# Kernel optimization log

Measured on AMD Instinct MI355X. Metric: run time of the kernel, lower is better.

The kernel has to match this reference:

```python
import jax, jax.numpy as jnp
import numpy as np

H_IN = 1024
H_OUT = 1024
P = 512
DT_MIN = 0.004
DT_MAX = 0.1
STEP_RESCALE = 1.0
MIN_NEG = 1e-3
EPS_LAM = 1e-6
EPS_DIV = 1e-9
CLIP_MAX = 20.0


def _hippo_lambda_raw(p):
    # Mirrors TorchS5.__init__ HiPPO-LegS-style symmetric init.
    idx = np.arange(p, dtype=np.float64)
    Pv = np.sqrt(1.0 + 2.0 * idx)
    A = np.tril(Pv[:, None] * Pv[None, :]) - np.diag(idx)
    A = -A
    Pr = np.sqrt(idx + 0.5)
    S = A + Pr[:, None] * Pr[None, :]
    S_sym = 0.5 * (S + S.T)
    eig = np.linalg.eigvalsh(S_sym).astype(np.float32)
    lambda_init = -np.clip(np.abs(eig), 1e-3, None)
    raw = -np.log(np.expm1(np.clip(-lambda_init, 1e-6, None)))
    return jnp.asarray(raw, dtype=jnp.float32)


def setup_inputs() -> dict:
    key = jax.random.key(0)
    ku, kt, kb, kc = jax.random.split(key, 4)
    Bsz, L = 16, 1024
    u = jax.random.normal(ku, (Bsz, L, H_IN), dtype=jnp.float32)
    timesteps = jax.random.uniform(kt, (Bsz, L), dtype=jnp.float32)
    Lambda_raw = _hippo_lambda_raw(P)
    log_step_init = 0.5 * (np.log(DT_MIN) + np.log(DT_MAX))
    log_step = jnp.full((P,), log_step_init, dtype=jnp.float32)
    # kaiming_uniform_(a=sqrt(5)) -> U(-1/sqrt(fan_in), 1/sqrt(fan_in))
    Bmat = jax.random.uniform(kb, (P, H_IN), dtype=jnp.float32,
                              minval=-1.0, maxval=1.0) / np.sqrt(H_IN)
    Cmat = jax.random.uniform(kc, (H_OUT, P), dtype=jnp.float32,
                              minval=-1.0, maxval=1.0) / np.sqrt(P)
    Dvec = jnp.zeros((H_IN,), dtype=jnp.float32)  # H_in == H_out path
    return {"u": u, "timesteps": timesteps, "Lambda_raw": Lambda_raw,
            "log_step": log_step, "B": Bmat, "C": Cmat, "D": Dvec}


def reference(u, timesteps, Lambda_raw, log_step, B, C, D):
    # u: [B,L,H_in], timesteps: [B,L]
    Bu = jnp.einsum('ph,blh->blp', B, u)                      # [B,L,P]
    step_vec = STEP_RESCALE * jnp.exp(log_step)               # [P]
    Lam = -(jax.nn.softplus(Lambda_raw) + MIN_NEG)            # [P]
    Delta = jnp.maximum(step_vec[None, None, :] * timesteps[..., None], 0.0)
    A_bar = jnp.exp(jnp.minimum(Lam[None, None, :] * Delta, CLIP_MAX))
    # zoh gamma: (exp(Lam*Delta)-1)/Lam, fallback Delta near Lam=0
    gamma = jnp.where(jnp.abs(Lam)[None, None, :] > EPS_LAM,
                      (A_bar - 1.0) / Lam[None, None, :], Delta)
    b_seq = gamma * Bu
    A_cum = jnp.cumprod(A_bar, axis=1)                        # [B,L,P]
    z = b_seq / (A_cum + EPS_DIV)
    s = jnp.cumsum(z, axis=1)
    x_seq = A_cum * s
    ys = jnp.einsum('hp,blp->blh', C, x_seq) + D * u          # [B,L,H_out]
    return ys
```

## Files before the change

kernel.cpp:

```cpp
#include <hip/hip_runtime.h>
#include <cstdint>
#include <cstddef>

#define H_IN   1024
#define H_OUTD 1024
#define PDIM   512
#define BSZ    16
#define LSEQ   1024
#define BLM    (BSZ * LSEQ)
#define CCH    32
#define CLEN   32

typedef __bf16 bf16_t;
typedef __bf16 bf16x8 __attribute__((ext_vector_type(8)));
typedef float  floatx4 __attribute__((ext_vector_type(4)));

__device__ __forceinline__ unsigned short f2bf(float f) {
    unsigned u = __float_as_uint(f);
    u = u + 0x7fffu + ((u >> 16) & 1u);
    return (unsigned short)(u >> 16);
}
__device__ __forceinline__ float bf2f(unsigned short s) {
    return __uint_as_float((unsigned)s << 16);
}

__device__ __forceinline__ void gl_lds16(const void* g, void* l) {
    __builtin_amdgcn_global_load_lds(
        (const __attribute__((address_space(1))) void*)g,
        (__attribute__((address_space(3))) void*)l, 16, 0, 0);
}

#define NU4 (BLM * H_IN / 4)
#define NB4 (PDIM * H_IN / 4)
#define NC4 (H_OUTD * PDIM / 4)
__global__ void setup_kernel(const float* __restrict__ Lraw,
                             const float* __restrict__ lstep,
                             float* __restrict__ stepv,
                             float* __restrict__ lamv,
                             const float4* __restrict__ Usrc,
                             ushort4* __restrict__ Udst,
                             const float4* __restrict__ Bsrc,
                             ushort4* __restrict__ Bdst,
                             const float4* __restrict__ Csrc,
                             ushort4* __restrict__ Cdst) {
    const int gid = blockIdx.x * 256 + threadIdx.x;
    if (gid < PDIM) {
        stepv[gid] = expf(lstep[gid]);
        float x = Lraw[gid];
        float sp = fmaxf(x, 0.0f) + log1pf(expf(-fabsf(x)));
        lamv[gid] = -(sp + 1e-3f);
    }
    if (gid < NU4) {
        float4 v = Usrc[gid];
        ushort4 o;
        o.x = f2bf(v.x); o.y = f2bf(v.y); o.z = f2bf(v.z); o.w = f2bf(v.w);
        Udst[gid] = o;
    } else {
        const int g2 = gid - NU4;
        if (g2 < NB4) {
            float4 v = Bsrc[g2];
            ushort4 o;
            o.x = f2bf(v.x); o.y = f2bf(v.y); o.z = f2bf(v.z); o.w = f2bf(v.w);
            Bdst[g2] = o;
        } else if (g2 < NB4 + NC4) {
            const int g3 = g2 - NB4;
            float4 v = Csrc[g3];
            ushort4 o;
            o.x = f2bf(v.x); o.y = f2bf(v.y); o.z = f2bf(v.z); o.w = f2bf(v.w);
            Cdst[g3] = o;
        }
    }
}

template<int GXL>
__global__ __launch_bounds__(256, 4)
void gemm1_bm64(const bf16_t* __restrict__ A, const bf16_t* __restrict__ Bm,
                unsigned short* __restrict__ Cb, int M, int N, int K) {
    constexpr int ABUF = 64 * 32;
    constexpr int BBUF = 128 * 32;
    __shared__ bf16_t As[2 * ABUF];
    __shared__ bf16_t Bs[2 * BBUF];

    const int i     = blockIdx.x;
    const int n_blk = (i >> 3) & ((1 << GXL) - 1);
    const int m_blk = ((i >> (3 + GXL)) << 3) | (i & 7);
    const int m0    = m_blk * 64;
    const int n0    = n_blk << 7;

    const int tid  = threadIdx.x;
    const int lane = tid & 63;
    const int w    = tid >> 6;
    const int wm   = (w & 1) * 32;
    const int wn   = (w >> 1) * 64;
    const int r16  = lane & 15;
    const int q    = lane >> 4;
    const int fsw  = (q ^ (r16 & 3)) << 3;

    const int srow = lane >> 2;
    const int seg  = (lane & 3) ^ (srow & 3);
    const int aro  = w * 16;
    const int bc0  = w * 32;

    const bf16_t* gA  = A  + (size_t)(m0 + aro + srow) * K + seg * 8;
    const bf16_t* gB0 = Bm + (size_t)(n0 + bc0 + srow) * K + seg * 8;
    const bf16_t* gB1 = Bm + (size_t)(n0 + bc0 + 16 + srow) * K + seg * 8;
    bf16_t* lA  = &As[aro * 32];
    bf16_t* lB0 = &Bs[bc0 * 32];
    bf16_t* lB1 = &Bs[(bc0 + 16) * 32];

    floatx4 acc[2][4] = {};

    gl_lds16(gA,  lA);
    gl_lds16(gB0, lB0);
    gl_lds16(gB1, lB1);
    __syncthreads();

    int cur = 0;
    for (int k0 = 0; k0 < K; k0 += 32) {
        const int nxt = cur ^ 1;
        if (k0 + 32 < K) {
            gl_lds16(gA  + k0 + 32, lA  + nxt * ABUF);
            gl_lds16(gB0 + k0 + 32, lB0 + nxt * BBUF);
            gl_lds16(gB1 + k0 + 32, lB1 + nxt * BBUF);
        }

        const bf16_t* rA = As + cur * ABUF;
        const bf16_t* rB = Bs + cur * BBUF;
        bf16x8 af[2], bfr[4];
#pragma unroll
        for (int ii = 0; ii < 2; ++ii)
            af[ii]  = *(const bf16x8*)&rA[(wm + ii * 16 + r16) * 32 + fsw];
#pragma unroll
        for (int ii = 0; ii < 4; ++ii)
            bfr[ii] = *(const bf16x8*)&rB[(wn + ii * 16 + r16) * 32 + fsw];
#pragma unroll
        for (int mi = 0; mi < 2; ++mi)
#pragma unroll
            for (int ni = 0; ni < 4; ++ni)
                acc[mi][ni] = __builtin_amdgcn_mfma_f32_16x16x32_bf16(
                    af[mi], bfr[ni], acc[mi][ni], 0, 0, 0);

        __syncthreads();
        cur = nxt;
    }

#pragma unroll
    for (int mi = 0; mi < 2; ++mi) {
#pragma unroll
        for (int e = 0; e < 4; ++e) {
            const int m = m0 + wm + mi * 16 + q * 4 + e;
#pragma unroll
            for (int ni = 0; ni < 4; ++ni) {
                const int n = n0 + wn + ni * 16 + r16;
                Cb[(size_t)m * N + n] = f2bf(acc[mi][ni][e]);
            }
        }
    }
}

template<int GXL>
__global__ __launch_bounds__(256, 4)
void gemm2_nt(const bf16_t* __restrict__ A, const bf16_t* __restrict__ Bm,
              float* __restrict__ Cf, int M, int N, int K,
              const float* __restrict__ Dv, const float* __restrict__ U32) {
    __shared__ bf16_t As[2 * 4096];
    __shared__ bf16_t Bs[2 * 4096];

    const int i     = blockIdx.x;
    const int n_blk = (i >> 3) & ((1 << GXL) - 1);
    const int m_blk = ((i >> (3 + GXL)) << 3) | (i & 7);
    const int m0    = m_blk << 7;
    const int n0    = n_blk << 7;

    const int tid  = threadIdx.x;
    const int lane = tid & 63;
    const int w    = tid >> 6;
    const int wm   = (w & 1) << 6;
    const int wn   = (w >> 1) << 6;
    const int r16  = lane & 15;
    const int q    = lane >> 4;
    const int fsw  = (q ^ (r16 & 3)) << 3;

    const int srow = lane >> 2;
    const int seg  = (lane & 3) ^ (srow & 3);
    const int c0   = w * 32;
    const int c1   = c0 + 16;

    const bf16_t* gA0 = A  + (size_t)(m0 + c0 + srow) * K + seg * 8;
    const bf16_t* gA1 = A  + (size_t)(m0 + c1 + srow) * K + seg * 8;
    const bf16_t* gB0 = Bm + (size_t)(n0 + c0 + srow) * K + seg * 8;
    const bf16_t* gB1 = Bm + (size_t)(n0 + c1 + srow) * K + seg * 8;
    bf16_t* lA0 = &As[c0 * 32];
    bf16_t* lA1 = &As[c1 * 32];
    bf16_t* lB0 = &Bs[c0 * 32];
    bf16_t* lB1 = &Bs[c1 * 32];

    floatx4 acc[4][4] = {};

    gl_lds16(gA0, lA0);
    gl_lds16(gA1, lA1);
    gl_lds16(gB0, lB0);
    gl_lds16(gB1, lB1);
    __syncthreads();

    int cur = 0;
    for (int k0 = 0; k0 < K; k0 += 32) {
        const int nxt = cur ^ 1;
        if (k0 + 32 < K) {
            gl_lds16(gA0 + k0 + 32, lA0 + nxt * 4096);
            gl_lds16(gA1 + k0 + 32, lA1 + nxt * 4096);
            gl_lds16(gB0 + k0 + 32, lB0 + nxt * 4096);
            gl_lds16(gB1 + k0 + 32, lB1 + nxt * 4096);
        }

        const bf16_t* rA = As + cur * 4096;
        const bf16_t* rB = Bs + cur * 4096;
        bf16x8 af[4], bfr[4];
#pragma unroll
        for (int ii = 0; ii < 4; ++ii) {
            af[ii]  = *(const bf16x8*)&rA[(wm + ii * 16 + r16) * 32 + fsw];
            bfr[ii] = *(const bf16x8*)&rB[(wn + ii * 16 + r16) * 32 + fsw];
        }
#pragma unroll
        for (int mi = 0; mi < 4; ++mi)
#pragma unroll
            for (int ni = 0; ni < 4; ++ni)
                acc[mi][ni] = __builtin_amdgcn_mfma_f32_16x16x32_bf16(
                    af[mi], bfr[ni], acc[mi][ni], 0, 0, 0);

        __syncthreads();
        cur = nxt;
    }

    float dn[4];
#pragma unroll
    for (int ni = 0; ni < 4; ++ni) dn[ni] = Dv[n0 + wn + ni * 16 + r16];
#pragma unroll
    for (int mi = 0; mi < 4; ++mi) {
#pragma unroll
        for (int e = 0; e < 4; ++e) {
            const int m = m0 + wm + mi * 16 + q * 4 + e;
#pragma unroll
            for (int ni = 0; ni < 4; ++ni) {
                const int n = n0 + wn + ni * 16 + r16;
                const size_t idx = (size_t)m * N + n;
                float v = acc[mi][ni][e];
                if (dn[ni] != 0.0f) v += dn[ni] * U32[idx];
                __builtin_nontemporal_store(v, &Cf[idx]);
            }
        }
    }
}

__global__ __launch_bounds__(512)
void scan_part1(const unsigned short* __restrict__ Bu, const float* __restrict__ ts,
                const float* __restrict__ stepv, const float* __restrict__ lamv,
                float* __restrict__ Pagg, float* __restrict__ Sagg) {
    const int c = blockIdx.x;
    const int b = blockIdx.y;
    const int p = threadIdx.x;

    const float lam  = lamv[p];
    const float stp  = stepv[p];
    const float rlam = 1.0f / lam;
    const bool  lam_big = fabsf(lam) > 1e-6f;

    const unsigned short* bu = Bu + ((size_t)b * LSEQ + c * CLEN) * PDIM + p;
    const float* tb = ts + b * LSEQ + c * CLEN;

    float P = 1.0f, S = 0.0f;
#pragma unroll 8
    for (int i = 0; i < CLEN; ++i) {
        float t     = tb[i];
        float delta = fmaxf(stp * t, 0.0f);
        float e     = fminf(lam * delta, 20.0f);
        float abar  = __expf(e);
        float gamma = lam_big ? (abar - 1.0f) * rlam : delta;
        S = fmaf(abar, S, gamma * bf2f(bu[(size_t)i * PDIM]));
        P *= abar;
    }
    const size_t o = ((size_t)b * CCH + c) * PDIM + p;
    Pagg[o] = P;
    Sagg[o] = S;
}

__global__ __launch_bounds__(512)
void scan_part23(const unsigned short* __restrict__ Bu, const float* __restrict__ ts,
                 const float* __restrict__ stepv, const float* __restrict__ lamv,
                 const float* __restrict__ Pagg, const float* __restrict__ Sagg,
                 unsigned short* __restrict__ Xbf) {
    const int c = blockIdx.x;
    const int b = blockIdx.y;
    const int p = threadIdx.x;

    const float lam  = lamv[p];
    const float stp  = stepv[p];
    const float rlam = 1.0f / lam;
    const bool  lam_big = fabsf(lam) > 1e-6f;

    const float* Pb = Pagg + (size_t)b * CCH * PDIM + p;
    const float* Sb = Sagg + (size_t)b * CCH * PDIM + p;
    float x = 0.0f;
    int cc = 0;
    for (; cc + 4 <= c; cc += 4) {
        float p0 = Pb[(size_t)(cc + 0) * PDIM], s0 = Sb[(size_t)(cc + 0) * PDIM];
        float p1 = Pb[(size_t)(cc + 1) * PDIM], s1 = Sb[(size_t)(cc + 1) * PDIM];
        float p2 = Pb[(size_t)(cc + 2) * PDIM], s2 = Sb[(size_t)(cc + 2) * PDIM];
        float p3 = Pb[(size_t)(cc + 3) * PDIM], s3 = Sb[(size_t)(cc + 3) * PDIM];
        float p01 = p0 * p1, s01 = fmaf(s0, p1, s1);
        float p23 = p2 * p3, s23 = fmaf(s2, p3, s3);
        float pq  = p01 * p23, sq = fmaf(s01, p23, s23);
        x = fmaf(pq, x, sq);
    }
    for (; cc < c; ++cc) {
        x = fmaf(Pb[(size_t)cc * PDIM], x, Sb[(size_t)cc * PDIM]);
    }

    const unsigned short* bu = Bu + ((size_t)b * LSEQ + c * CLEN) * PDIM + p;
    const float* tb = ts + b * LSEQ + c * CLEN;
    unsigned short* xo = Xbf + ((size_t)b * LSEQ + c * CLEN) * PDIM + p;

#pragma unroll 8
    for (int i = 0; i < CLEN; ++i) {
        float t     = tb[i];
        float delta = fmaxf(stp * t, 0.0f);
        float e     = fminf(lam * delta, 20.0f);
        float abar  = __expf(e);
        float gamma = lam_big ? (abar - 1.0f) * rlam : delta;
        x = fmaf(abar, x, gamma * bf2f(bu[(size_t)i * PDIM]));
        xo[(size_t)i * PDIM] = f2bf(x);
    }
}

extern "C" void kernel_launch(void* const* d_in, const int* in_sizes, int n_in,
                              void* d_out, int out_size, void* d_ws, size_t ws_size,
                              hipStream_t stream) {
    (void)in_sizes; (void)n_in; (void)out_size; (void)ws_size;
    const float* u  = (const float*)d_in[0];
    const float* ts = (const float*)d_in[1];
    const float* Lr = (const float*)d_in[2];
    const float* ls = (const float*)d_in[3];
    const float* Bm = (const float*)d_in[4];
    const float* Cm = (const float*)d_in[5];
    const float* Dv = (const float*)d_in[6];
    float* out = (float*)d_out;

    char* ws = (char*)d_ws;
    bf16_t*         u_bf = (bf16_t*)(ws);
    bf16_t*         B_bf = (bf16_t*)(ws + (32u << 20));
    bf16_t*         C_bf = (bf16_t*)(ws + (33u << 20));
    unsigned short* Bu   = (unsigned short*)(ws + (34u << 20));
    unsigned short* X_bf = (unsigned short*)(ws + (50u << 20));
    float*          Pagg = (float*)(ws + (66u << 20));
    float*          Sagg = (float*)(ws + (67u << 20));
    float*          stepv= (float*)(ws + (69u << 20));
    float*          lamv = stepv + PDIM;

    setup_kernel<<<(NU4 + NB4 + NC4) / 256, 256, 0, stream>>>(
        Lr, ls, stepv, lamv,
        (const float4*)u,  (ushort4*)u_bf,
        (const float4*)Bm, (ushort4*)B_bf,
        (const float4*)Cm, (ushort4*)C_bf);

    gemm1_bm64<2><<<1024, 256, 0, stream>>>(
        u_bf, B_bf, Bu, BLM, PDIM, H_IN);

    scan_part1<<<dim3(CCH, BSZ), 512, 0, stream>>>(Bu, ts, stepv, lamv, Pagg, Sagg);
    scan_part23<<<dim3(CCH, BSZ), 512, 0, stream>>>(Bu, ts, stepv, lamv,
                                                    Pagg, Sagg, X_bf);

    gemm2_nt<3><<<1024, 256, 0, stream>>>(
        (const bf16_t*)X_bf, C_bf, out, BLM, H_OUTD, PDIM, Dv, u);
}
```

Baseline: 195.6 us.

## Use 128x128 tiles with 8 waves in gemm1, change LDS swizzle, drop nontemporal stores

The first GEMM moves from 64x128 tiles with 4 waves to 128x128 tiles with 8 waves. Each wave now computes a 64x32 sub-tile, and the grid is halved. This raises data reuse per block and cuts redundant global loads of B. Both GEMMs get a new LDS XOR swizzle intended to reduce bank conflicts, and the output stores in gemm2 become regular stores instead of nontemporal ones. The larger block could lower occupancy or leave fewer blocks to balance across CUs.

```diff
diff --git a/kernel.cpp b/kernel.cpp
--- a/kernel.cpp
+++ b/kernel.cpp
@@ -73,70 +73,63 @@
 }
 
 template<int GXL>
-__global__ __launch_bounds__(256, 4)
-void gemm1_bm64(const bf16_t* __restrict__ A, const bf16_t* __restrict__ Bm,
-                unsigned short* __restrict__ Cb, int M, int N, int K) {
-    constexpr int ABUF = 64 * 32;
-    constexpr int BBUF = 128 * 32;
-    __shared__ bf16_t As[2 * ABUF];
-    __shared__ bf16_t Bs[2 * BBUF];
+__global__ __launch_bounds__(512, 4)
+void gemm1_8w(const bf16_t* __restrict__ A, const bf16_t* __restrict__ Bm,
+              unsigned short* __restrict__ Cb, int M, int N, int K) {
+    __shared__ bf16_t As[2 * 4096];
+    __shared__ bf16_t Bs[2 * 4096];
 
     const int i     = blockIdx.x;
     const int n_blk = (i >> 3) & ((1 << GXL) - 1);
     const int m_blk = ((i >> (3 + GXL)) << 3) | (i & 7);
-    const int m0    = m_blk * 64;
+    const int m0    = m_blk << 7;
     const int n0    = n_blk << 7;
 
     const int tid  = threadIdx.x;
     const int lane = tid & 63;
     const int w    = tid >> 6;
-    const int wm   = (w & 1) * 32;
-    const int wn   = (w >> 1) * 64;
+    const int wm   = (w & 1) << 6;
+    const int wn   = (w >> 1) << 5;
     const int r16  = lane & 15;
     const int q    = lane >> 4;
-    const int fsw  = (q ^ (r16 & 3)) << 3;
+    const int fsw  = ((q ^ ((r16 + (r16 >> 2)) & 3)) << 3);
 
     const int srow = lane >> 2;
-    const int seg  = (lane & 3) ^ (srow & 3);
-    const int aro  = w * 16;
-    const int bc0  = w * 32;
-
-    const bf16_t* gA  = A  + (size_t)(m0 + aro + srow) * K + seg * 8;
-    const bf16_t* gB0 = Bm + (size_t)(n0 + bc0 + srow) * K + seg * 8;
-    const bf16_t* gB1 = Bm + (size_t)(n0 + bc0 + 16 + srow) * K + seg * 8;
-    bf16_t* lA  = &As[aro * 32];
-    bf16_t* lB0 = &Bs[bc0 * 32];
-    bf16_t* lB1 = &Bs[(bc0 + 16) * 32];
-
-    floatx4 acc[2][4] = {};
-
-    gl_lds16(gA,  lA);
-    gl_lds16(gB0, lB0);
-    gl_lds16(gB1, lB1);
+    const int seg  = (lane & 3) ^ ((srow + (srow >> 2)) & 3);
+    const int cw   = w << 4;
+
+    const bf16_t* gA = A  + (size_t)(m0 + cw + srow) * K + seg * 8;
+    const bf16_t* gB = Bm + (size_t)(n0 + cw + srow) * K + seg * 8;
+    bf16_t* lA = &As[cw * 32];
+    bf16_t* lB = &Bs[cw * 32];
+
+    floatx4 acc[4][2] = {};
+
+    gl_lds16(gA, lA);
+    gl_lds16(gB, lB);
     __syncthreads();
 
     int cur = 0;
     for (int k0 = 0; k0 < K; k0 += 32) {
         const int nxt = cur ^ 1;
         if (k0 + 32 < K) {
-            gl_lds16(gA  + k0 + 32, lA  + nxt * ABUF);
-            gl_lds16(gB0 + k0 + 32, lB0 + nxt * BBUF);
-            gl_lds16(gB1 + k0 + 32, lB1 + nxt * BBUF);
-        }
-
-        const bf16_t* rA = As + cur * ABUF;
-        const bf16_t* rB = Bs + cur * BBUF;
-        bf16x8 af[2], bfr[4];
+            gl_lds16(gA + k0 + 32, lA + nxt * 4096);
+            gl_lds16(gB + k0 + 32, lB + nxt * 4096);
+        }
+
+        const bf16_t* rA = As + cur * 4096;
+        const bf16_t* rB = Bs + cur * 4096;
+        bf16x8 af[4], bfr[2];
+#pragma unroll
+        for (int ii = 0; ii < 4; ++ii)
+            af[ii]  = *(const bf16x8*)&rA[(wm + ii * 16 + r16) * 32 + fsw];
 #pragma unroll
         for (int ii = 0; ii < 2; ++ii)
-            af[ii]  = *(const bf16x8*)&rA[(wm + ii * 16 + r16) * 32 + fsw];
-#pragma unroll
-        for (int ii = 0; ii < 4; ++ii)
             bfr[ii] = *(const bf16x8*)&rB[(wn + ii * 16 + r16) * 32 + fsw];
 #pragma unroll
-        for (int mi = 0; mi < 2; ++mi)
-#pragma unroll
-            for (int ni = 0; ni < 4; ++ni)
+        for (int mi = 0; mi < 4; ++mi)
+#pragma unroll
+            for (int ni = 0; ni < 2; ++ni)
                 acc[mi][ni] = __builtin_amdgcn_mfma_f32_16x16x32_bf16(
                     af[mi], bfr[ni], acc[mi][ni], 0, 0, 0);
 
@@ -145,12 +138,12 @@
     }
 
 #pragma unroll
-    for (int mi = 0; mi < 2; ++mi) {
+    for (int mi = 0; mi < 4; ++mi) {
 #pragma unroll
         for (int e = 0; e < 4; ++e) {
             const int m = m0 + wm + mi * 16 + q * 4 + e;
 #pragma unroll
-            for (int ni = 0; ni < 4; ++ni) {
+            for (int ni = 0; ni < 2; ++ni) {
                 const int n = n0 + wn + ni * 16 + r16;
                 Cb[(size_t)m * N + n] = f2bf(acc[mi][ni][e]);
             }
@@ -179,10 +172,10 @@
     const int wn   = (w >> 1) << 6;
     const int r16  = lane & 15;
     const int q    = lane >> 4;
-    const int fsw  = (q ^ (r16 & 3)) << 3;
+    const int fsw  = ((q ^ ((r16 + (r16 >> 2)) & 3)) << 3);
 
     const int srow = lane >> 2;
-    const int seg  = (lane & 3) ^ (srow & 3);
+    const int seg  = (lane & 3) ^ ((srow + (srow >> 2)) & 3);
     const int c0   = w * 32;
     const int c1   = c0 + 16;
 
@@ -246,7 +239,7 @@
                 const size_t idx = (size_t)m * N + n;
                 float v = acc[mi][ni][e];
                 if (dn[ni] != 0.0f) v += dn[ni] * U32[idx];
-                __builtin_nontemporal_store(v, &Cf[idx]);
+                Cf[idx] = v;
             }
         }
     }
@@ -362,7 +355,7 @@
         (const float4*)Bm, (ushort4*)B_bf,
         (const float4*)Cm, (ushort4*)C_bf);
 
-    gemm1_bm64<2><<<1024, 256, 0, stream>>>(
+    gemm1_8w<2><<<512, 512, 0, stream>>>(
         u_bf, B_bf, Bu, BLM, PDIM, H_IN);
 
     scan_part1<<<dim3(CCH, BSZ), 512, 0, stream>>>(Bu, ts, stepv, lamv, Pagg, Sagg);
```

Measured after the change: 186.1 us. 4.8% less time.
